# Kernel optimization log

Measured on AMD Instinct MI355X. Metric: run time of the kernel, lower is better.

## Reference

```python
import jax, jax.numpy as jnp
import numpy as np

N_USER = 100000
N_ITEM = 50000
N_NODES = N_USER + N_ITEM
EMB = 64
NNZ = 4000000
BATCH = 4096
N_LAYERS = 3  # len(eval(args.layer_size)) with layer_size=[64,64,64]


def setup_inputs() -> dict:
    key = jax.random.key(0)
    k = jax.random.split(key, 8)
    adj_rows = jax.random.randint(k[0], (NNZ,), 0, N_NODES, dtype=jnp.int32)
    adj_cols = jax.random.randint(k[1], (NNZ,), 0, N_NODES, dtype=jnp.int32)
    adj_vals = jax.random.uniform(k[2], (NNZ,), dtype=jnp.float32)
    user_emb = jax.random.normal(k[3], (N_USER, EMB), dtype=jnp.float32)
    item_emb = jax.random.normal(k[4], (N_ITEM, EMB), dtype=jnp.float32)
    users = jax.random.randint(k[5], (BATCH,), 0, N_USER, dtype=jnp.int32)
    pos_items = jax.random.randint(k[6], (BATCH,), 0, N_ITEM, dtype=jnp.int32)
    neg_items = jax.random.randint(k[7], (BATCH,), 0, N_ITEM, dtype=jnp.int32)
    return {
        "adj_rows": adj_rows, "adj_cols": adj_cols, "adj_vals": adj_vals,
        "user_emb": user_emb, "item_emb": item_emb,
        "users": users, "pos_items": pos_items, "neg_items": neg_items,
    }


def _spmm(rows, cols, vals, x):
    # sparse [N,N] @ dense [N,D] via gather + segment-sum (COO)
    gathered = vals[:, None] * x[cols]          # [nnz, D]
    return jax.ops.segment_sum(gathered, rows, num_segments=N_NODES)


def reference(adj_rows, adj_cols, adj_vals, user_emb, item_emb,
              users, pos_items, neg_items):
    ego = jnp.concatenate([user_emb, item_emb], axis=0)  # [N, D]
    # Source quirk: ego_embeddings is never updated in the layer loop, so
    # every layer appends the same A_hat @ ego; mean over [ego] + L copies.
    prop = _spmm(adj_rows, adj_cols, adj_vals, ego)      # [N, D]
    light_out = (ego + N_LAYERS * prop) / (N_LAYERS + 1)
    u_g = light_out[:N_USER]
    i_g = light_out[N_USER:]
    out = jnp.stack([u_g[users], i_g[pos_items], i_g[neg_items]], axis=0)
    return out  # [3, BATCH, EMB]
```

## Files before the change

kernel.cpp:

```cpp
#include <hip/hip_runtime.h>

#define N_USER 100000
#define N_ITEM 50000
#define N_NODES 150000
#define EMB 64
#define NNZ 4000000
#define BATCH 4096

#define PROP_OFF 150016

__global__ void mark_zero_kernel(const int* __restrict__ users,
                                 const int* __restrict__ pos_items,
                                 const int* __restrict__ neg_items,
                                 unsigned char* __restrict__ flags,
                                 float* __restrict__ prop) {
    int t = blockIdx.x * blockDim.x + threadIdx.x;
    int wave = t >> 6;
    int lane = t & 63;
    int k = wave >> 12;
    int i = wave & 4095;
    int node;
    if (k == 0)      node = users[i];
    else if (k == 1) node = N_USER + pos_items[i];
    else             node = N_USER + neg_items[i];
    prop[(size_t)node * EMB + lane] = 0.0f;
    if (lane == 0) flags[node] = 1;
}

__global__ void spmm_kernel(const int* __restrict__ rows,
                            const int* __restrict__ cols,
                            const float* __restrict__ vals,
                            const float* __restrict__ user_emb,
                            const float* __restrict__ item_emb,
                            const unsigned char* __restrict__ flags,
                            float* __restrict__ prop) {
    int tid = blockIdx.x * blockDim.x + threadIdx.x;
    int lane = threadIdx.x & 63;
    int row = rows[tid];
    int col = cols[tid];
    float val = vals[tid];
    bool needed = flags[row] != 0;
    unsigned long long mask = __ballot(needed);
    while (mask) {
        int src = __ffsll((unsigned long long)mask) - 1;
        mask &= mask - 1;
        int r = __builtin_amdgcn_readlane(row, src);
        int c = __builtin_amdgcn_readlane(col, src);
        float v = __uint_as_float(__builtin_amdgcn_readlane(__float_as_uint(val), src));
        const float* x = (c < N_USER) ? (user_emb + (size_t)c * EMB)
                                      : (item_emb + (size_t)(c - N_USER) * EMB);
        atomicAdd(prop + (size_t)r * EMB + lane, v * x[lane]);
    }
}

__global__ void gather_kernel(const int* __restrict__ users,
                              const int* __restrict__ pos_items,
                              const int* __restrict__ neg_items,
                              const float* __restrict__ user_emb,
                              const float* __restrict__ item_emb,
                              const float* __restrict__ prop,
                              float* __restrict__ out) {
    int t = blockIdx.x * blockDim.x + threadIdx.x;
    int wave = t >> 6;
    int lane = t & 63;
    int k = wave >> 12;
    int i = wave & 4095;
    int node;
    if (k == 0)      node = users[i];
    else if (k == 1) node = N_USER + pos_items[i];
    else             node = N_USER + neg_items[i];
    float ego = (node < N_USER)
                    ? user_emb[(size_t)node * EMB + lane]
                    : item_emb[(size_t)(node - N_USER) * EMB + lane];
    float p = prop[(size_t)node * EMB + lane];
    out[t] = (ego + 3.0f * p) * 0.25f;
}

extern "C" void kernel_launch(void* const* d_in, const int* in_sizes, int n_in,
                              void* d_out, int out_size, void* d_ws, size_t ws_size,
                              hipStream_t stream) {
    const int*   adj_rows = (const int*)  d_in[0];
    const int*   adj_cols = (const int*)  d_in[1];
    const float* adj_vals = (const float*)d_in[2];
    const float* user_emb = (const float*)d_in[3];
    const float* item_emb = (const float*)d_in[4];
    const int*   users    = (const int*)  d_in[5];
    const int*   pos      = (const int*)  d_in[6];
    const int*   neg      = (const int*)  d_in[7];
    float* out = (float*)d_out;

    unsigned char* flags = (unsigned char*)d_ws;
    float* prop = (float*)((char*)d_ws + PROP_OFF);

    hipMemsetAsync(flags, 0, N_NODES, stream);

    mark_zero_kernel<<<3072, 256, 0, stream>>>(users, pos, neg, flags, prop);

    spmm_kernel<<<15625, 256, 0, stream>>>(adj_rows, adj_cols, adj_vals,
                                           user_emb, item_emb, flags, prop);

    gather_kernel<<<3072, 256, 0, stream>>>(users, pos, neg,
                                            user_emb, item_emb, prop, out);
}
```

Before: 190.4 us.

## Use bitmask row filter, compact needed edges, process four edges per wave

Replaces the byte flag array with a bit mask, so the per-edge membership lookup touches a table small enough to stay in cache. In the SpMM, lanes holding needed edges are compacted with ds_permute, and each wave handles four edges at once using 16 lanes and float4 loads per edge, in place of one edge per 64-lane iteration. The mark and gather kernels are vectorised to float4 with a quarter of the threads. The cost is more shuffle and permute instructions per wave, and the bit mask is now set with atomicOr.

New measurement: 402.7 us. +111.5%, slower.

```diff
diff --git a/kernel.cpp b/kernel.cpp
--- a/kernel.cpp
+++ b/kernel.cpp
@@ -6,25 +6,27 @@
 #define EMB 64
 #define NNZ 4000000
 #define BATCH 4096
+#define NSLOTS (3 * BATCH)
 
-#define PROP_OFF 150016
+#define BM_OFF   0
+#define PROP_OFF 19200
 
-__global__ void mark_zero_kernel(const int* __restrict__ users,
-                                 const int* __restrict__ pos_items,
-                                 const int* __restrict__ neg_items,
-                                 unsigned char* __restrict__ flags,
-                                 float* __restrict__ prop) {
+__global__ void mark_kernel(const int* __restrict__ users,
+                            const int* __restrict__ pos_items,
+                            const int* __restrict__ neg_items,
+                            unsigned int* __restrict__ bitmask,
+                            float* __restrict__ prop) {
     int t = blockIdx.x * blockDim.x + threadIdx.x;
-    int wave = t >> 6;
-    int lane = t & 63;
-    int k = wave >> 12;
-    int i = wave & 4095;
+    int slot = t >> 4;
+    int sub = t & 15;
+    int k = slot >> 12;
+    int i = slot & 4095;
     int node;
     if (k == 0)      node = users[i];
     else if (k == 1) node = N_USER + pos_items[i];
     else             node = N_USER + neg_items[i];
-    prop[(size_t)node * EMB + lane] = 0.0f;
-    if (lane == 0) flags[node] = 1;
+    ((float4*)(prop + (size_t)node * EMB))[sub] = make_float4(0.f, 0.f, 0.f, 0.f);
+    if (sub == 0) atomicOr(bitmask + (node >> 5), 1u << (node & 31));
 }
 
 __global__ void spmm_kernel(const int* __restrict__ rows,
@@ -32,24 +34,48 @@
                             const float* __restrict__ vals,
                             const float* __restrict__ user_emb,
                             const float* __restrict__ item_emb,
-                            const unsigned char* __restrict__ flags,
+                            const unsigned int* __restrict__ bitmask,
                             float* __restrict__ prop) {
     int tid = blockIdx.x * blockDim.x + threadIdx.x;
     int lane = threadIdx.x & 63;
     int row = rows[tid];
     int col = cols[tid];
     float val = vals[tid];
-    bool needed = flags[row] != 0;
+
+    unsigned int w = bitmask[row >> 5];
+    bool needed = (w >> (row & 31)) & 1;
     unsigned long long mask = __ballot(needed);
-    while (mask) {
-        int src = __ffsll((unsigned long long)mask) - 1;
-        mask &= mask - 1;
-        int r = __builtin_amdgcn_readlane(row, src);
-        int c = __builtin_amdgcn_readlane(col, src);
-        float v = __uint_as_float(__builtin_amdgcn_readlane(__float_as_uint(val), src));
-        const float* x = (c < N_USER) ? (user_emb + (size_t)c * EMB)
-                                      : (item_emb + (size_t)(c - N_USER) * EMB);
-        atomicAdd(prop + (size_t)r * EMB + lane, v * x[lane]);
+    if (mask == 0ull) return;
+    int cnt = __popcll(mask);
+
+    unsigned long long before = mask & ((1ull << lane) - 1ull);
+    int nb = __popcll(before);
+    int pos = needed ? nb : cnt + (lane - nb);
+    int addr = pos << 2;
+    int cr = __builtin_amdgcn_ds_permute(addr, row);
+    int cc = __builtin_amdgcn_ds_permute(addr, col);
+    int cv = __builtin_amdgcn_ds_permute(addr, __float_as_int(val));
+
+    int group = lane >> 4;
+    int gl = lane & 15;
+    for (int j = 0; j < cnt; j += 4) {
+        int e = j + group;
+        bool valid = e < cnt;
+        int ee = valid ? e : 0;
+        int r = __shfl(cr, ee);
+        int c = __shfl(cc, ee);
+        float v = __int_as_float(__shfl(cv, ee));
+        if (valid) {
+            const float4* x = (const float4*)((c < N_USER)
+                                ? user_emb + (size_t)c * EMB
+                                : item_emb + (size_t)(c - N_USER) * EMB);
+            float4 xv = x[gl];
+            float* p = prop + (size_t)r * EMB + gl * 4;
+            atomicAdd(p + 0, v * xv.x);
+            atomicAdd(p + 1, v * xv.y);
+            atomicAdd(p + 2, v * xv.z);
+            atomicAdd(p + 3, v * xv.w);
+        }
     }
 }
 
@@ -61,19 +87,25 @@
                               const float* __restrict__ prop,
                               float* __restrict__ out) {
     int t = blockIdx.x * blockDim.x + threadIdx.x;
-    int wave = t >> 6;
-    int lane = t & 63;
-    int k = wave >> 12;
-    int i = wave & 4095;
+    int slot = t >> 4;
+    int sub = t & 15;
+    int k = slot >> 12;
+    int i = slot & 4095;
     int node;
     if (k == 0)      node = users[i];
     else if (k == 1) node = N_USER + pos_items[i];
     else             node = N_USER + neg_items[i];
-    float ego = (node < N_USER)
-                    ? user_emb[(size_t)node * EMB + lane]
-                    : item_emb[(size_t)(node - N_USER) * EMB + lane];
-    float p = prop[(size_t)node * EMB + lane];
-    out[t] = (ego + 3.0f * p) * 0.25f;
+    const float4* ego = (const float4*)((node < N_USER)
+                          ? user_emb + (size_t)node * EMB
+                          : item_emb + (size_t)(node - N_USER) * EMB);
+    float4 e = ego[sub];
+    float4 p = ((const float4*)(prop + (size_t)node * EMB))[sub];
+    float4 o;
+    o.x = (e.x + 3.0f * p.x) * 0.25f;
+    o.y = (e.y + 3.0f * p.y) * 0.25f;
+    o.z = (e.z + 3.0f * p.z) * 0.25f;
+    o.w = (e.w + 3.0f * p.w) * 0.25f;
+    ((float4*)out)[t] = o;
 }
 
 extern "C" void kernel_launch(void* const* d_in, const int* in_sizes, int n_in,
@@ -89,16 +121,16 @@
     const int*   neg      = (const int*)  d_in[7];
     float* out = (float*)d_out;
 
-    unsigned char* flags = (unsigned char*)d_ws;
-    float* prop = (float*)((char*)d_ws + PROP_OFF);
+    unsigned int* bitmask = (unsigned int*)((char*)d_ws + BM_OFF);
+    float*        prop    = (float*)       ((char*)d_ws + PROP_OFF);
 
-    hipMemsetAsync(flags, 0, N_NODES, stream);
+    hipMemsetAsync(bitmask, 0, 18752, stream);
 
-    mark_zero_kernel<<<3072, 256, 0, stream>>>(users, pos, neg, flags, prop);
+    mark_kernel<<<768, 256, 0, stream>>>(users, pos, neg, bitmask, prop);
 
     spmm_kernel<<<15625, 256, 0, stream>>>(adj_rows, adj_cols, adj_vals,
-                                           user_emb, item_emb, flags, prop);
+                                           user_emb, item_emb, bitmask, prop);
 
-    gather_kernel<<<3072, 256, 0, stream>>>(users, pos, neg,
-                                            user_emb, item_emb, prop, out);
+    gather_kernel<<<768, 256, 0, stream>>>(users, pos, neg,
+                                           user_emb, item_emb, prop, out);
 }
```
